# Optimization experiments

Hardware: AMD Instinct MI355X
Metric: run time of the kernel (lower is better)

## Reference

```python
import jax, jax.numpy as jnp
import numpy as np

B, N, EM = 16, 1024, 768
D_K, D_V, H = 768, 768, 12

def setup_inputs() -> dict:
    key = jax.random.key(0)
    ks = jax.random.split(key, 4)
    s = 0.02
    x = jax.random.normal(ks[0], (B, N, EM), dtype=jnp.float32)
    W_qk = jax.random.normal(ks[1], (EM, 2 * D_K), dtype=jnp.float32) * s
    b_qk = jnp.zeros((2 * D_K,), dtype=jnp.float32)
    W_v = jax.random.normal(ks[2], (EM, D_V), dtype=jnp.float32) * s
    b_v = jnp.zeros((D_V,), dtype=jnp.float32)
    W_proj = jax.random.normal(ks[3], (D_V, EM), dtype=jnp.float32) * s
    b_proj = jnp.zeros((EM,), dtype=jnp.float32)
    return {"x": x, "W_qk": W_qk, "b_qk": b_qk, "W_v": W_v, "b_v": b_v,
            "W_proj": W_proj, "b_proj": b_proj}

def reference(x, W_qk, b_qk, W_v, b_v, W_proj, b_proj):
    b, n, _ = x.shape
    d = D_K // H  # per-head dim
    # qk Linear -> [B,N,2*d_K]; rearrange 'b n (h d qk) -> qk b h n d'
    # i.e. last dim splits as (h, d, 2) with qk fastest-varying.
    qk = (x @ W_qk + b_qk).reshape(b, n, H, d, 2)
    Q = jnp.transpose(qk[..., 0], (0, 2, 1, 3))  # [B,H,N,d]
    K = jnp.transpose(qk[..., 1], (0, 2, 1, 3))  # [B,H,N,d]
    V = (x @ W_v + b_v).reshape(b, n, H, D_V // H).transpose(0, 2, 1, 3)  # [B,H,N,dv]
    scores = jnp.einsum('bhqd,bhkd->bhqk', Q, K) / jnp.sqrt(jnp.float32(d))
    att = jax.nn.softmax(scores, axis=-1)  # dropout p=0 -> identity
    out = jnp.einsum('bhqk,bhkv->bhqv', att, V)  # [B,H,N,dv]
    out = out.transpose(0, 2, 1, 3).reshape(b, n, D_V)
    return out @ W_proj + b_proj
```

## Files before the change

kernel.cpp:

```cpp
#include <hip/hip_runtime.h>
#include <hip/hip_bf16.h>
#include <stdint.h>

typedef unsigned short u16;
typedef __bf16 bf16_t;
typedef bf16_t bf16x8 __attribute__((ext_vector_type(8)));
typedef short s16x4 __attribute__((ext_vector_type(4)));
typedef float f32x4 __attribute__((ext_vector_type(4)));

__device__ __forceinline__ u16 f2bf(float f) {
    union { float f; uint32_t i; } v; v.f = f;
    uint32_t i = v.i;
    uint32_t r = (i + 0x7FFFu + ((i >> 16) & 1u)) >> 16;
    return (u16)r;
}

__device__ __forceinline__ void gload_lds16(const u16* g, u16* l) {
    auto gp = (const __attribute__((address_space(1))) void*)g;
    auto lp = (__attribute__((address_space(3))) void*)(uintptr_t)l;
    __builtin_amdgcn_global_load_lds(gp, lp, 16, 0, 0);
}

__global__ void prep_kernel(const float* __restrict__ x, u16* __restrict__ xb,
                            const float* __restrict__ Wqk, const float* __restrict__ bqk,
                            u16* __restrict__ Wqkt, float* __restrict__ bqkp,
                            const float* __restrict__ Wv, u16* __restrict__ Wvt,
                            const float* __restrict__ Wp, u16* __restrict__ Wpt) {
    int id = blockIdx.x;
    if (id < 12288) {
        int i = id * 256 + threadIdx.x;
        float4 v = ((const float4*)x)[i];
        ushort4 o;
        o.x = f2bf(v.x); o.y = f2bf(v.y); o.z = f2bf(v.z); o.w = f2bf(v.w);
        ((ushort4*)xb)[i] = o;
    } else if (id < 13056) {
        int k = id - 12288;
        const float* row = Wqk + (size_t)k * 1536;
        for (int c = threadIdx.x; c < 1536; c += 256) {
            int qk = c & 1;
            int r  = qk * 768 + (c >> 7) * 64 + ((c >> 1) & 63);
            float s = qk ? 1.0f : 0.125f;
            Wqkt[(size_t)r * 768 + k] = f2bf(s * row[c]);
        }
        if (k == 0) {
            for (int c = threadIdx.x; c < 1536; c += 256) {
                int qk = c & 1;
                int r  = qk * 768 + (c >> 7) * 64 + ((c >> 1) & 63);
                bqkp[r] = (qk ? 1.0f : 0.125f) * bqk[c];
            }
        }
    } else {
        int sid = id - 13056;
        const float* W = (sid < 768) ? Wv : Wp;
        u16* Wt        = (sid < 768) ? Wvt : Wpt;
        int k = (sid < 768) ? sid : (sid - 768);
        const float* row = W + (size_t)k * 768;
        for (int n = threadIdx.x; n < 768; n += 256)
            Wt[(size_t)n * 768 + k] = f2bf(row[n]);
    }
}

__global__ __launch_bounds__(256)
void gemm_qkv_kernel(const u16* __restrict__ A,
                     const u16* __restrict__ Wqkt, const u16* __restrict__ Wvt,
                     const float* __restrict__ bqkp, const float* __restrict__ bv,
                     u16* __restrict__ Qp, u16* __restrict__ Kp, u16* __restrict__ Vp) {
    __shared__ __attribute__((aligned(16))) u16 As[2][128 * 64];
    __shared__ __attribute__((aligned(16))) u16 Bs[2][128 * 64];
    const int K = 768;

    const int tid  = threadIdx.x;
    const int lane = tid & 63;
    const int wave = tid >> 6;
    const int l16  = lane & 15;
    const int quad = lane >> 4;
    const int cpx  = 2304 >> 3;
    const int swz  = ((int)blockIdx.x & 7) * cpx + ((int)blockIdx.x >> 3);
    const int mt   = swz / 18;
    const int nt   = swz % 18;
    const bool vmode = nt >= 12;
    const int m0 = mt * 128;
    const int n0 = (vmode ? nt - 12 : nt) * 128;
    const u16* Bt = vmode ? Wvt : Wqkt;
    const float* bias = vmode ? bv : bqkp;
    const int wm = (wave & 1) * 64;
    const int wn = (wave >> 1) * 64;

    f32x4 acc[4][4];
#pragma unroll
    for (int i = 0; i < 4; i++)
#pragma unroll
        for (int j = 0; j < 4; j++) acc[i][j] = (f32x4){0.f, 0.f, 0.f, 0.f};

    const int rs   = lane >> 3;
    const int gseg = (lane & 7) ^ rs;
    const u16* Ag[4]; const u16* Bg[4];
#pragma unroll
    for (int c = 0; c < 4; c++) {
        Ag[c] = A  + (size_t)(m0 + c * 32 + wave * 8 + rs) * K + gseg * 8;
        Bg[c] = Bt + (size_t)(n0 + c * 32 + wave * 8 + rs) * K + gseg * 8;
    }
    const int sw7 = l16 & 7;

#pragma unroll
    for (int c = 0; c < 4; c++) {
        gload_lds16(Ag[c], &As[0][wave * 512 + c * 2048]);
        gload_lds16(Bg[c], &Bs[0][wave * 512 + c * 2048]);
    }

    int cur = 0;
    for (int t = 0; t < 12; ++t) {
        __syncthreads();
        if (t < 11) {
#pragma unroll
            for (int c = 0; c < 4; c++) {
                gload_lds16(Ag[c] + (t + 1) * 64, &As[cur ^ 1][wave * 512 + c * 2048]);
                gload_lds16(Bg[c] + (t + 1) * 64, &Bs[cur ^ 1][wave * 512 + c * 2048]);
            }
        }
        const u16* Asc = As[cur];
        const u16* Bsc = Bs[cur];

        bf16x8 af[4][2], bfr[4][2];
#pragma unroll
        for (int i = 0; i < 4; i++) {
#pragma unroll
            for (int hh = 0; hh < 2; hh++) {
                af[i][hh]  = *(const bf16x8*)&Asc[(wm + i * 16 + l16) * 64 +
                                                  (((hh * 4 + quad) ^ sw7) * 8)];
                bfr[i][hh] = *(const bf16x8*)&Bsc[(wn + i * 16 + l16) * 64 +
                                                  (((hh * 4 + quad) ^ sw7) * 8)];
            }
        }
        __builtin_amdgcn_s_setprio(1);
        if (vmode) {
#pragma unroll
            for (int i = 0; i < 4; i++)
#pragma unroll
                for (int j = 0; j < 4; j++)
#pragma unroll
                    for (int hh = 0; hh < 2; hh++)
                        acc[i][j] = __builtin_amdgcn_mfma_f32_16x16x32_bf16(af[i][hh], bfr[j][hh], acc[i][j], 0, 0, 0);
        } else {
#pragma unroll
            for (int i = 0; i < 4; i++)
#pragma unroll
                for (int j = 0; j < 4; j++)
#pragma unroll
                    for (int hh = 0; hh < 2; hh++)
                        acc[i][j] = __builtin_amdgcn_mfma_f32_16x16x32_bf16(bfr[j][hh], af[i][hh], acc[i][j], 0, 0, 0);
        }
        __builtin_amdgcn_s_setprio(0);
        cur ^= 1;
    }

    if (vmode) {
#pragma unroll
        for (int j = 0; j < 4; j++) {
            int cnb = n0 + wn + j * 16;
            int h   = cnb >> 6;
            int dv  = (cnb & 63) + l16;
            float bvv = bias[cnb + l16];
#pragma unroll
            for (int i = 0; i < 4; i++) {
                int cm = m0 + wm + i * 16 + quad * 4;
                int bb = cm >> 10, n = cm & 1023;
                ushort4 o;
                o.x = f2bf(acc[i][j][0] + bvv);
                o.y = f2bf(acc[i][j][1] + bvv);
                o.z = f2bf(acc[i][j][2] + bvv);
                o.w = f2bf(acc[i][j][3] + bvv);
                *(ushort4*)&Vp[((size_t)((bb * 12 + h) * 64 + dv)) * 1024 + n] = o;
            }
        }
    } else {
#pragma unroll
        for (int j = 0; j < 4; j++) {
            int f0 = n0 + wn + j * 16 + quad * 4;
            float4 bv4 = *(const float4*)&bias[f0];
            int qk = f0 >= 768;
            int hd = f0 - qk * 768;
            int h  = hd >> 6;
            int d0 = hd & 63;
            u16* dst = qk ? Kp : Qp;
#pragma unroll
            for (int i = 0; i < 4; i++) {
                int t = m0 + wm + i * 16 + l16;
                int bb = t >> 10, n = t & 1023;
                ushort4 o;
                o.x = f2bf(acc[i][j][0] + bv4.x);
                o.y = f2bf(acc[i][j][1] + bv4.y);
                o.z = f2bf(acc[i][j][2] + bv4.z);
                o.w = f2bf(acc[i][j][3] + bv4.w);
                *(ushort4*)&dst[((size_t)((bb * 12 + h) * 1024 + n)) * 64 + d0] = o;
            }
        }
    }
}

__global__ __launch_bounds__(256)
void gemm_out_kernel(const u16* __restrict__ A, const u16* __restrict__ Bt,
                     const float* __restrict__ bias, float* __restrict__ Cout,
                     int M, int N, int K) {
    __shared__ __attribute__((aligned(16))) u16 As[2][128 * 64];
    __shared__ __attribute__((aligned(16))) u16 Bs[2][128 * 64];

    const int tid  = threadIdx.x;
    const int lane = tid & 63;
    const int wave = tid >> 6;
    const int l16  = lane & 15;
    const int quad = lane >> 4;
    const int nxt = N >> 7;
    const int cpx = (int)gridDim.x >> 3;
    const int swz = ((int)blockIdx.x & 7) * cpx + ((int)blockIdx.x >> 3);
    const int m0 = (swz / nxt) * 128;
    const int n0 = (swz % nxt) * 128;
    const int wm = (wave & 1) * 64;
    const int wn = (wave >> 1) * 64;

    f32x4 acc[4][4];
#pragma unroll
    for (int i = 0; i < 4; i++)
#pragma unroll
        for (int j = 0; j < 4; j++) acc[i][j] = (f32x4){0.f, 0.f, 0.f, 0.f};

    const int rs   = lane >> 3;
    const int gseg = (lane & 7) ^ rs;
    const u16* Ag[4]; const u16* Bg[4];
#pragma unroll
    for (int c = 0; c < 4; c++) {
        Ag[c] = A  + (size_t)(m0 + c * 32 + wave * 8 + rs) * K + gseg * 8;
        Bg[c] = Bt + (size_t)(n0 + c * 32 + wave * 8 + rs) * K + gseg * 8;
    }
    const int sw7 = l16 & 7;
    const int nk = K >> 6;

#pragma unroll
    for (int c = 0; c < 4; c++) {
        gload_lds16(Ag[c], &As[0][wave * 512 + c * 2048]);
        gload_lds16(Bg[c], &Bs[0][wave * 512 + c * 2048]);
    }

    int cur = 0;
    for (int t = 0; t < nk; ++t) {
        __syncthreads();
        if (t < nk - 1) {
#pragma unroll
            for (int c = 0; c < 4; c++) {
                gload_lds16(Ag[c] + (t + 1) * 64, &As[cur ^ 1][wave * 512 + c * 2048]);
                gload_lds16(Bg[c] + (t + 1) * 64, &Bs[cur ^ 1][wave * 512 + c * 2048]);
            }
        }
        const u16* Asc = As[cur];
        const u16* Bsc = Bs[cur];

        bf16x8 af[4][2], bfr[4][2];
#pragma unroll
        for (int i = 0; i < 4; i++) {
#pragma unroll
            for (int hh = 0; hh < 2; hh++) {
                af[i][hh]  = *(const bf16x8*)&Asc[(wm + i * 16 + l16) * 64 +
                                                  (((hh * 4 + quad) ^ sw7) * 8)];
                bfr[i][hh] = *(const bf16x8*)&Bsc[(wn + i * 16 + l16) * 64 +
                                                  (((hh * 4 + quad) ^ sw7) * 8)];
            }
        }
        __builtin_amdgcn_s_setprio(1);
#pragma unroll
        for (int i = 0; i < 4; i++)
#pragma unroll
            for (int j = 0; j < 4; j++)
#pragma unroll
                for (int hh = 0; hh < 2; hh++)
                    acc[i][j] = __builtin_amdgcn_mfma_f32_16x16x32_bf16(bfr[j][hh], af[i][hh], acc[i][j], 0, 0, 0);
        __builtin_amdgcn_s_setprio(0);
        cur ^= 1;
    }

#pragma unroll
    for (int j = 0; j < 4; j++) {
        int f0 = n0 + wn + j * 16 + quad * 4;
        float4 bv = *(const float4*)&bias[f0];
#pragma unroll
        for (int i = 0; i < 4; i++) {
            int t = m0 + wm + i * 16 + l16;
            float4 o;
            o.x = acc[i][j][0] + bv.x;
            o.y = acc[i][j][1] + bv.y;
            o.z = acc[i][j][2] + bv.z;
            o.w = acc[i][j][3] + bv.w;
            *(float4*)&Cout[(size_t)t * N + f0] = o;
        }
    }
}

__global__ __launch_bounds__(512)
void attention_mfma_kernel(const u16* __restrict__ Qp, const u16* __restrict__ Kp,
                           const u16* __restrict__ Vp, u16* __restrict__ attout) {
    __shared__ __attribute__((aligned(16))) u16 Ks[2][64 * 64];
    __shared__ __attribute__((aligned(16))) u16 Vs[2][64 * 64];

    const int tid  = threadIdx.x;
    const int wave = tid >> 6;
    const int lane = tid & 63;
    const int l16  = lane & 15;
    const int quad = lane >> 4;
    const int flat = blockIdx.x;
    const int swz  = (flat & 7) * 96 + (flat >> 3);
    const int bh   = swz >> 2;
    const int b    = bh / 12, h = bh % 12;
    const int q0   = (swz & 3) * 256 + wave * 32;

    const u16* Qhead = Qp + (size_t)bh * 1024 * 64;
    const u16* Khead = Kp + (size_t)bh * 1024 * 64;
    const u16* Vhead = Vp + (size_t)bh * 64 * 1024;

    bf16x8 qf[2][2];
#pragma unroll
    for (int qb = 0; qb < 2; qb++) {
        const u16* qrow = Qhead + (size_t)(q0 + qb * 16 + l16) * 64;
        qf[qb][0] = *(const bf16x8*)(qrow + quad * 8);
        qf[qb][1] = *(const bf16x8*)(qrow + 32 + quad * 8);
    }

    f32x4 oacc[2][4];
#pragma unroll
    for (int qb = 0; qb < 2; qb++)
#pragma unroll
        for (int db = 0; db < 4; db++) oacc[qb][db] = (f32x4){0.f, 0.f, 0.f, 0.f};
    float l_part[2] = {0.f, 0.f};

    const int srow = tid >> 3;
    const int gseg = (tid & 7) ^ (srow & 7);
    const u16* Kg = Khead + (size_t)srow * 64 + gseg * 8;
    const u16* Vg = Vhead + (size_t)srow * 1024 + gseg * 8;
    const int sw7 = l16 & 7;

    gload_lds16(Kg, &Ks[0][wave * 512]);
    gload_lds16(Vg, &Vs[0][wave * 512]);

    int cur = 0;
    for (int t = 0; t < 16; ++t) {
        __syncthreads();
        if (t < 15) {
            gload_lds16(Kg + (t + 1) * 4096, &Ks[cur ^ 1][wave * 512]);
            gload_lds16(Vg + (t + 1) * 64,   &Vs[cur ^ 1][wave * 512]);
        }
        const u16* Ksc = Ks[cur];
        const u16* Vsc = Vs[cur];

        union { uint32_t u[4]; bf16x8 v; } pf8[2][2];
        {
            bf16x8 kf[4][2];
#pragma unroll
            for (int jb = 0; jb < 4; jb++) {
#pragma unroll
                for (int hf = 0; hf < 2; hf++)
                    kf[jb][hf] = *(const bf16x8*)&Ksc[(jb * 16 + l16) * 64 +
                                                      (((hf * 4 + quad) ^ sw7) * 8)];
            }
#pragma unroll
            for (int qb = 0; qb < 2; qb++) {
#pragma unroll
                for (int jb = 0; jb < 4; jb++) {
                    f32x4 st = (f32x4){0.f, 0.f, 0.f, 0.f};
                    __builtin_amdgcn_s_setprio(1);
                    st = __builtin_amdgcn_mfma_f32_16x16x32_bf16(kf[jb][0], qf[qb][0], st, 0, 0, 0);
                    st = __builtin_amdgcn_mfma_f32_16x16x32_bf16(kf[jb][1], qf[qb][1], st, 0, 0, 0);
                    __builtin_amdgcn_s_setprio(0);
                    float e0 = __expf(st[0]), e1 = __expf(st[1]);
                    float e2 = __expf(st[2]), e3 = __expf(st[3]);
                    l_part[qb] += (e0 + e1) + (e2 + e3);
                    union { __hip_bfloat162 h2; uint32_t u; } c0, c1;
                    c0.h2 = __float22bfloat162_rn(make_float2(e0, e1));
                    c1.h2 = __float22bfloat162_rn(make_float2(e2, e3));
                    pf8[qb][jb >> 1].u[(jb & 1) * 2 + 0] = c0.u;
                    pf8[qb][jb >> 1].u[(jb & 1) * 2 + 1] = c1.u;
                }
            }
        }

        __builtin_amdgcn_s_setprio(1);
#pragma unroll
        for (int db = 0; db < 4; db++) {
#pragma unroll
            for (int jp = 0; jp < 2; jp++) {
                union { s16x4 hh[2]; bf16x8 v; } vb8;
                int glo = 4 * jp + (quad >> 1);
                int ghi = glo + 2;
                vb8.hh[0] = *(const s16x4*)&Vsc[(db * 16 + l16) * 64 +
                                                ((glo ^ sw7) * 8) + (quad & 1) * 4];
                vb8.hh[1] = *(const s16x4*)&Vsc[(db * 16 + l16) * 64 +
                                                ((ghi ^ sw7) * 8) + (quad & 1) * 4];
#pragma unroll
                for (int qb = 0; qb < 2; qb++)
                    oacc[qb][db] = __builtin_amdgcn_mfma_f32_16x16x32_bf16(
                        pf8[qb][jp].v, vb8.v, oacc[qb][db], 0, 0, 0);
            }
        }
        __builtin_amdgcn_s_setprio(0);
        cur ^= 1;
    }

#pragma unroll
    for (int qb = 0; qb < 2; qb++) {
        float l = l_part[qb];
        l += __shfl_xor(l, 16);
        l += __shfl_xor(l, 32);
        float linv[4];
#pragma unroll
        for (int r = 0; r < 4; r++)
            linv[r] = 1.0f / __shfl(l, quad * 4 + r);
        u16* orow = attout + (size_t)(b * 1024 + q0 + qb * 16 + quad * 4) * 768 + h * 64 + l16;
#pragma unroll
        for (int db = 0; db < 4; db++)
#pragma unroll
            for (int r = 0; r < 4; r++)
                orow[(size_t)r * 768 + db * 16] = f2bf(oacc[qb][db][r] * linv[r]);
    }
}

extern "C" void kernel_launch(void* const* d_in, const int* in_sizes, int n_in,
                              void* d_out, int out_size, void* d_ws, size_t ws_size,
                              hipStream_t stream) {
    const float* x      = (const float*)d_in[0];
    const float* W_qk   = (const float*)d_in[1];
    const float* b_qk   = (const float*)d_in[2];
    const float* W_v    = (const float*)d_in[3];
    const float* b_v    = (const float*)d_in[4];
    const float* W_proj = (const float*)d_in[5];
    const float* b_proj = (const float*)d_in[6];
    float* out = (float*)d_out;

    char* ws = (char*)d_ws;
    size_t off = 0;
    auto alloc = [&](size_t bytes) { void* p = ws + off; off += (bytes + 255) & ~255ull; return p; };
    u16*   xb     = (u16*)alloc((size_t)16384 * 768 * 2);
    u16*   Wqkt   = (u16*)alloc((size_t)1536 * 768 * 2);
    float* bqkp   = (float*)alloc(1536 * 4);
    u16*   Wvt    = (u16*)alloc((size_t)768 * 768 * 2);
    u16*   Wprojt = (u16*)alloc((size_t)768 * 768 * 2);
    u16*   Qp     = (u16*)alloc((size_t)16384 * 768 * 2);
    u16*   Kp     = (u16*)alloc((size_t)16384 * 768 * 2);
    u16*   Vp     = (u16*)alloc((size_t)16384 * 768 * 2);
    u16*   attout = (u16*)alloc((size_t)16384 * 768 * 2);

    prep_kernel<<<14592, 256, 0, stream>>>(x, xb, W_qk, b_qk, Wqkt, bqkp,
                                           W_v, Wvt, W_proj, Wprojt);

    gemm_qkv_kernel<<<2304, 256, 0, stream>>>(xb, Wqkt, Wvt, bqkp, b_v, Qp, Kp, Vp);
    attention_mfma_kernel<<<768, 512, 0, stream>>>(Qp, Kp, Vp, attout);
    gemm_out_kernel<<<768, 256, 0, stream>>>(attout, Wprojt, b_proj, out, 16384, 768, 768);
}
```

Before: 327.6 us.

## Enlarge GEMM tiles to 256x128 with 8 waves and triple-buffered LDS pipeline

Both projection GEMMs move from 128x128 tiles with 4 waves to 256x128 tiles with 8 waves. Global-to-LDS loads now use a three-stage ring that prefetches two k-steps ahead, synchronised with explicit vmcnt waits and raw barriers. The aim is more reuse of the B tile, fewer blocks, and better hiding of load latency. LDS use rises to 144 KB per block, which limits residency. Each wave still computes a 64x64 sub-tile.

```diff
diff --git a/kernel.cpp b/kernel.cpp
--- a/kernel.cpp
+++ b/kernel.cpp
@@ -60,13 +60,13 @@
     }
 }
 
-__global__ __launch_bounds__(256)
+__global__ __launch_bounds__(512, 2)
 void gemm_qkv_kernel(const u16* __restrict__ A,
                      const u16* __restrict__ Wqkt, const u16* __restrict__ Wvt,
                      const float* __restrict__ bqkp, const float* __restrict__ bv,
                      u16* __restrict__ Qp, u16* __restrict__ Kp, u16* __restrict__ Vp) {
-    __shared__ __attribute__((aligned(16))) u16 As[2][128 * 64];
-    __shared__ __attribute__((aligned(16))) u16 Bs[2][128 * 64];
+    __shared__ __attribute__((aligned(16))) u16 As[3][256 * 64];
+    __shared__ __attribute__((aligned(16))) u16 Bs[3][128 * 64];
     const int K = 768;
 
     const int tid  = threadIdx.x;
@@ -74,17 +74,17 @@
     const int wave = tid >> 6;
     const int l16  = lane & 15;
     const int quad = lane >> 4;
-    const int cpx  = 2304 >> 3;
+    const int cpx  = 1152 >> 3;
     const int swz  = ((int)blockIdx.x & 7) * cpx + ((int)blockIdx.x >> 3);
     const int mt   = swz / 18;
     const int nt   = swz % 18;
     const bool vmode = nt >= 12;
-    const int m0 = mt * 128;
+    const int m0 = mt * 256;
     const int n0 = (vmode ? nt - 12 : nt) * 128;
     const u16* Bt = vmode ? Wvt : Wqkt;
     const float* bias = vmode ? bv : bqkp;
-    const int wm = (wave & 1) * 64;
-    const int wn = (wave >> 1) * 64;
+    const int wm = (wave >> 1) * 64;
+    const int wn = (wave & 1) * 64;
 
     f32x4 acc[4][4];
 #pragma unroll
@@ -94,32 +94,35 @@
 
     const int rs   = lane >> 3;
     const int gseg = (lane & 7) ^ rs;
-    const u16* Ag[4]; const u16* Bg[4];
-#pragma unroll
-    for (int c = 0; c < 4; c++) {
-        Ag[c] = A  + (size_t)(m0 + c * 32 + wave * 8 + rs) * K + gseg * 8;
-        Bg[c] = Bt + (size_t)(n0 + c * 32 + wave * 8 + rs) * K + gseg * 8;
-    }
+    const u16* Ag[4]; const u16* Bg[2];
+#pragma unroll
+    for (int c = 0; c < 4; c++)
+        Ag[c] = A + (size_t)(m0 + c * 64 + wave * 8 + rs) * K + gseg * 8;
+#pragma unroll
+    for (int c = 0; c < 2; c++)
+        Bg[c] = Bt + (size_t)(n0 + c * 64 + wave * 8 + rs) * K + gseg * 8;
     const int sw7 = l16 & 7;
 
-#pragma unroll
-    for (int c = 0; c < 4; c++) {
-        gload_lds16(Ag[c], &As[0][wave * 512 + c * 2048]);
-        gload_lds16(Bg[c], &Bs[0][wave * 512 + c * 2048]);
-    }
-
-    int cur = 0;
+    auto stage = [&](int t, int buf) {
+#pragma unroll
+        for (int c = 0; c < 4; c++)
+            gload_lds16(Ag[c] + t * 64, &As[buf][c * 4096 + wave * 512]);
+#pragma unroll
+        for (int c = 0; c < 2; c++)
+            gload_lds16(Bg[c] + t * 64, &Bs[buf][c * 4096 + wave * 512]);
+    };
+
+    stage(0, 0);
+    stage(1, 1);
+
     for (int t = 0; t < 12; ++t) {
-        __syncthreads();
-        if (t < 11) {
-#pragma unroll
-            for (int c = 0; c < 4; c++) {
-                gload_lds16(Ag[c] + (t + 1) * 64, &As[cur ^ 1][wave * 512 + c * 2048]);
-                gload_lds16(Bg[c] + (t + 1) * 64, &Bs[cur ^ 1][wave * 512 + c * 2048]);
-            }
-        }
-        const u16* Asc = As[cur];
-        const u16* Bsc = Bs[cur];
+        if (t < 11) asm volatile("s_waitcnt vmcnt(6)" ::: "memory");
+        else        asm volatile("s_waitcnt vmcnt(0)" ::: "memory");
+        __builtin_amdgcn_s_barrier();
+        __builtin_amdgcn_sched_barrier(0);
+        if (t + 2 < 12) stage(t + 2, (t + 2) % 3);
+        const u16* Asc = As[t % 3];
+        const u16* Bsc = Bs[t % 3];
 
         bf16x8 af[4][2], bfr[4][2];
 #pragma unroll
@@ -151,7 +154,6 @@
                         acc[i][j] = __builtin_amdgcn_mfma_f32_16x16x32_bf16(bfr[j][hh], af[i][hh], acc[i][j], 0, 0, 0);
         }
         __builtin_amdgcn_s_setprio(0);
-        cur ^= 1;
     }
 
     if (vmode) {
@@ -198,12 +200,12 @@
     }
 }
 
-__global__ __launch_bounds__(256)
+__global__ __launch_bounds__(512, 2)
 void gemm_out_kernel(const u16* __restrict__ A, const u16* __restrict__ Bt,
                      const float* __restrict__ bias, float* __restrict__ Cout,
                      int M, int N, int K) {
-    __shared__ __attribute__((aligned(16))) u16 As[2][128 * 64];
-    __shared__ __attribute__((aligned(16))) u16 Bs[2][128 * 64];
+    __shared__ __attribute__((aligned(16))) u16 As[3][256 * 64];
+    __shared__ __attribute__((aligned(16))) u16 Bs[3][128 * 64];
 
     const int tid  = threadIdx.x;
     const int lane = tid & 63;
@@ -213,10 +215,10 @@
     const int nxt = N >> 7;
     const int cpx = (int)gridDim.x >> 3;
     const int swz = ((int)blockIdx.x & 7) * cpx + ((int)blockIdx.x >> 3);
-    const int m0 = (swz / nxt) * 128;
+    const int m0 = (swz / nxt) * 256;
     const int n0 = (swz % nxt) * 128;
-    const int wm = (wave & 1) * 64;
-    const int wn = (wave >> 1) * 64;
+    const int wm = (wave >> 1) * 64;
+    const int wn = (wave & 1) * 64;
 
     f32x4 acc[4][4];
 #pragma unroll
@@ -226,33 +228,36 @@
 
     const int rs   = lane >> 3;
     const int gseg = (lane & 7) ^ rs;
-    const u16* Ag[4]; const u16* Bg[4];
-#pragma unroll
-    for (int c = 0; c < 4; c++) {
-        Ag[c] = A  + (size_t)(m0 + c * 32 + wave * 8 + rs) * K + gseg * 8;
-        Bg[c] = Bt + (size_t)(n0 + c * 32 + wave * 8 + rs) * K + gseg * 8;
-    }
+    const u16* Ag[4]; const u16* Bg[2];
+#pragma unroll
+    for (int c = 0; c < 4; c++)
+        Ag[c] = A + (size_t)(m0 + c * 64 + wave * 8 + rs) * K + gseg * 8;
+#pragma unroll
+    for (int c = 0; c < 2; c++)
+        Bg[c] = Bt + (size_t)(n0 + c * 64 + wave * 8 + rs) * K + gseg * 8;
     const int sw7 = l16 & 7;
     const int nk = K >> 6;
 
-#pragma unroll
-    for (int c = 0; c < 4; c++) {
-        gload_lds16(Ag[c], &As[0][wave * 512 + c * 2048]);
-        gload_lds16(Bg[c], &Bs[0][wave * 512 + c * 2048]);
-    }
-
-    int cur = 0;
+    auto stage = [&](int t, int buf) {
+#pragma unroll
+        for (int c = 0; c < 4; c++)
+            gload_lds16(Ag[c] + t * 64, &As[buf][c * 4096 + wave * 512]);
+#pragma unroll
+        for (int c = 0; c < 2; c++)
+            gload_lds16(Bg[c] + t * 64, &Bs[buf][c * 4096 + wave * 512]);
+    };
+
+    stage(0, 0);
+    stage(1, 1);
+
     for (int t = 0; t < nk; ++t) {
-        __syncthreads();
-        if (t < nk - 1) {
-#pragma unroll
-            for (int c = 0; c < 4; c++) {
-                gload_lds16(Ag[c] + (t + 1) * 64, &As[cur ^ 1][wave * 512 + c * 2048]);
-                gload_lds16(Bg[c] + (t + 1) * 64, &Bs[cur ^ 1][wave * 512 + c * 2048]);
-            }
-        }
-        const u16* Asc = As[cur];
-        const u16* Bsc = Bs[cur];
+        if (t < nk - 1) asm volatile("s_waitcnt vmcnt(6)" ::: "memory");
+        else            asm volatile("s_waitcnt vmcnt(0)" ::: "memory");
+        __builtin_amdgcn_s_barrier();
+        __builtin_amdgcn_sched_barrier(0);
+        if (t + 2 < nk) stage(t + 2, (t + 2) % 3);
+        const u16* Asc = As[t % 3];
+        const u16* Bsc = Bs[t % 3];
 
         bf16x8 af[4][2], bfr[4][2];
 #pragma unroll
@@ -274,7 +279,6 @@
                 for (int hh = 0; hh < 2; hh++)
                     acc[i][j] = __builtin_amdgcn_mfma_f32_16x16x32_bf16(bfr[j][hh], af[i][hh], acc[i][j], 0, 0, 0);
         __builtin_amdgcn_s_setprio(0);
-        cur ^= 1;
     }
 
 #pragma unroll
@@ -448,7 +452,7 @@
     prep_kernel<<<14592, 256, 0, stream>>>(x, xb, W_qk, b_qk, Wqkt, bqkp,
                                            W_v, Wvt, W_proj, Wprojt);
 
-    gemm_qkv_kernel<<<2304, 256, 0, stream>>>(xb, Wqkt, Wvt, bqkp, b_v, Qp, Kp, Vp);
+    gemm_qkv_kernel<<<1152, 512, 0, stream>>>(xb, Wqkt, Wvt, bqkp, b_v, Qp, Kp, Vp);
     attention_mfma_kernel<<<768, 512, 0, stream>>>(Qp, Kp, Vp, attout);
-    gemm_out_kernel<<<768, 256, 0, stream>>>(attout, Wprojt, b_proj, out, 16384, 768, 768);
-}
+    gemm_out_kernel<<<384, 512, 0, stream>>>(attout, Wprojt, b_proj, out, 16384, 768, 768);
+}
```

After: 345.8 us. 1.06x slower.
